# Kernel tuning notes

Hardware: AMD Instinct MI355X
Metric: run time of the kernel (lower is better)

## Reference

```python
import jax, jax.numpy as jnp
import numpy as np

B, N, F, E, K, R, H = 16, 2048, 2048, 128, 10, 2, 2


def setup_inputs() -> dict:
    key = jax.random.key(0)
    ks = jax.random.split(key, 11)
    s = 0.1  # keep embeddings close so the Gaussian kernel does not underflow
    rel = jax.random.normal(ks[0], (B, E), jnp.float32) * s
    arg1 = jax.random.normal(ks[1], (B, E), jnp.float32) * s
    arg2 = jax.random.normal(ks[2], (B, E), jnp.float32) * s
    fact_rel = jax.random.normal(ks[3], (B, F, E), jnp.float32) * s
    fact_arg1 = jax.random.normal(ks[4], (B, F, E), jnp.float32) * s
    fact_arg2 = jax.random.normal(ks[5], (B, F, E), jnp.float32) * s
    entity_embeddings = jax.random.normal(ks[6], (B, N, E), jnp.float32) * s
    hop_W = jax.random.normal(ks[7], (R, H, E, E), jnp.float32) / jnp.sqrt(jnp.float32(E))
    hop_b = jax.random.normal(ks[8], (R, H, E), jnp.float32) * 0.01
    nb_facts = jax.random.randint(ks[9], (B,), F // 2, F + 1, jnp.int32)
    nb_entities = jax.random.randint(ks[10], (B,), N // 2, N + 1, jnp.int32)
    return dict(rel=rel, arg1=arg1, arg2=arg2, fact_rel=fact_rel,
                fact_arg1=fact_arg1, fact_arg2=fact_arg2,
                entity_embeddings=entity_embeddings, hop_W=hop_W, hop_b=hop_b,
                nb_facts=nb_facts, nb_entities=nb_entities)


def reference(rel, arg1, arg2, fact_rel, fact_arg1, fact_arg2,
              entity_embeddings, hop_W, hop_b, nb_facts, nb_entities):
    # Gaussian kernel k(x,y) = exp(-||x-y||^2 / 2), batched: x [B,T,E], y [B,F,E] -> [B,T,F]
    def kern(x, y):
        d2 = (jnp.sum(x * x, -1)[:, :, None] + jnp.sum(y * y, -1)[:, None, :]
              - 2.0 * jnp.einsum('bte,bfe->btf', x, y))
        return jnp.exp(-0.5 * d2)

    fact_mask = (jnp.arange(F) < nb_facts[:, None])[:, None, :]            # [B,1,F]
    ent_mask = (jnp.arange(N) < nb_entities[:, None]).astype(rel.dtype)    # [B,N]

    # BatchNeuralKB.score: max over (valid) facts of product of kernels. [B,T,E]x3 -> [B,T]
    def model_score(r, a1, a2):
        s = kern(r, fact_rel) * kern(a1, fact_arg1) * kern(a2, fact_arg2)  # [B,T,F]
        return jnp.max(jnp.where(fact_mask, s, 0.0), axis=-1)

    # BatchNeuralKB.forward, (s,p,?) -> score per candidate object entity. [B,1,E] -> [B,N]
    def forward_sp(r, a1):
        kr = jnp.where(fact_mask, kern(r, fact_rel) * kern(a1, fact_arg1), 0.0)  # [B,1,F]
        kE = kern(entity_embeddings, fact_arg2)                                  # [B,N,F]
        return jnp.max(kr * kE, axis=-1) * ent_mask                              # [B,N]

    # (?,p,o) -> score per candidate subject entity
    def forward_po(r, a2):
        kr = jnp.where(fact_mask, kern(r, fact_rel) * kern(a2, fact_arg2), 0.0)
        kE = kern(entity_embeddings, fact_arg1)
        return jnp.max(kr * kE, axis=-1) * ent_mask

    # r_score(depth=1) = max(depth_r_score(0), depth_r_score(1))
    # depth_r_score(0) == model.score
    scores_0 = model_score(rel[:, None], arg1[:, None], arg2[:, None])[:, 0]  # [B]

    global_res = None
    for r_idx in range(R):
        is_rev = (r_idx % 2 == 1)
        # LinearReformulator: hop relations from rel
        h1 = rel @ hop_W[r_idx, 0] + hop_b[r_idx, 0]  # [B,E]
        h2 = rel @ hop_W[r_idx, 1] + hop_b[r_idx, 1]
        # hop 1: r_hop -> scores over all entities, then top-k beam
        if is_rev:
            sp = forward_po(h1[:, None], arg1[:, None])  # [B,N]
        else:
            sp = forward_sp(h1[:, None], arg1[:, None])
        z_scores, z_idx = jax.lax.top_k(sp, K)                                  # [B,K]
        z_emb = jnp.take_along_axis(entity_embeddings, z_idx[:, :, None], axis=1)  # [B,K,E]
        # final hop: r_score(depth=0) == model.score with branched args
        h2k = jnp.broadcast_to(h2[:, None, :], (B, K, E))
        a2k = jnp.broadcast_to(arg2[:, None, :], (B, K, E))
        if is_rev:
            s2 = model_score(h2k, a2k, z_emb)  # [B,K]
        else:
            s2 = model_score(h2k, z_emb, a2k)
        rule_scores = jnp.minimum(s2, z_scores)   # tnorm = 'min'
        rule_res = jnp.max(rule_scores, axis=1)   # max over branches [B]
        global_res = rule_res if global_res is None else jnp.maximum(global_res, rule_res)

    return jnp.maximum(scores_0, global_res)
```

## Files before the change

### kernel.cpp

```cpp
#include <hip/hip_runtime.h>
#include <math.h>

#define Bb 16
#define Nn 2048
#define Ff 2048
#define Ee 128
#define Kk 10
#define S2FC 8
#define S2F (Ff / S2FC)

typedef __attribute__((ext_vector_type(8))) short short8;
typedef __attribute__((ext_vector_type(4))) float f32x4;

__device__ inline float wave_sum(float x) {
    for (int o = 32; o; o >>= 1) x += __shfl_down(x, o);
    return x;
}

__device__ inline void bsplit(float x, unsigned short& h, unsigned short& l) {
    unsigned int u = __float_as_uint(x);
    h = (unsigned short)(u >> 16);
    float hf = __uint_as_float(u & 0xFFFF0000u);
    l = (unsigned short)(__float_as_uint(x - hf) >> 16);
}

__device__ inline void atomic_fmax_pos(float* addr, float v) {
    atomicMax((unsigned int*)addr, __float_as_uint(v));
}

__global__ __launch_bounds__(256) void k_pfe(
    const float* __restrict__ rel, const float* __restrict__ arg1,
    const float* __restrict__ arg2, const float* __restrict__ frel,
    const float* __restrict__ fa1, const float* __restrict__ fa2,
    const float* __restrict__ ent, const float* __restrict__ hop_W,
    const float* __restrict__ hop_b, const int* __restrict__ nb_facts,
    unsigned short* __restrict__ B0, unsigned short* __restrict__ B1,
    float* __restrict__ ent_norm, float* __restrict__ c0, float* __restrict__ c1,
    float* __restrict__ s2b0, float* __restrict__ s2b1, float* __restrict__ out) {
    int bx = blockIdx.x;
    int tid = threadIdx.x;
    if (bx < 128) {
        int fcb = bx & 7, b = bx >> 3;
        int nbf = nb_facts[b];
        if (fcb * 256 >= nbf) {
            int f = fcb * 256 + tid;
            size_t o = (size_t)b * Ff + f;
            const float NI = -INFINITY;
            c0[o] = NI; c1[o] = NI; s2b0[o] = NI; s2b1[o] = NI;
            return;
        }
        __shared__ float q[7][Ee];
        __shared__ float bred[4];
        if (tid < 128) {
            q[0][tid] = rel[b * Ee + tid];
            q[1][tid] = arg1[b * Ee + tid];
            q[2][tid] = arg2[b * Ee + tid];
        }
        __syncthreads();
        {
            int e = tid & 127, hf = tid >> 7;
            const float* W0 = hop_W + (size_t)(hf * 2) * Ee * Ee;
            const float* W1 = W0 + (size_t)Ee * Ee;
            float a0 = hop_b[(hf * 2) * Ee + e];
            float a1 = hop_b[(hf * 2 + 1) * Ee + e];
            for (int qq = 0; qq < Ee; ++qq) {
                float rq = q[0][qq];
                a0 += rq * W0[qq * Ee + e];
                a1 += rq * W1[qq * Ee + e];
            }
            q[3 + hf][e] = a0;
            q[5 + hf][e] = a1;
        }
        __syncthreads();

        int f = fcb * 256 + tid;
        const float* pr = frel + ((size_t)b * Ff + f) * Ee;
        const float* p1 = fa1 + ((size_t)b * Ff + f) * Ee;
        const float* p2 = fa2 + ((size_t)b * Ff + f) * Ee;
        float d_rr = 0, d_a11 = 0, d_a22 = 0, d_h10 = 0, d_h11 = 0, d_h20 = 0, d_h21 = 0;
        float d_a12 = 0, d_a21 = 0, n1 = 0, n2 = 0;
#pragma unroll 8
        for (int e0 = 0; e0 < Ee; e0 += 4) {
            float4 vr4 = *(const float4*)(pr + e0);
            float4 v14 = *(const float4*)(p1 + e0);
            float4 v24 = *(const float4*)(p2 + e0);
            const float* vrp = (const float*)&vr4;
            const float* v1p = (const float*)&v14;
            const float* v2p = (const float*)&v24;
#pragma unroll
            for (int j = 0; j < 4; ++j) {
                int e = e0 + j;
                float fr = vrp[j], f1 = v1p[j], f2 = v2p[j];
                float t;
                t = q[0][e] - fr; d_rr  += t * t;
                t = q[1][e] - f1; d_a11 += t * t;
                t = q[2][e] - f2; d_a22 += t * t;
                t = q[3][e] - fr; d_h10 += t * t;
                t = q[4][e] - fr; d_h11 += t * t;
                t = q[5][e] - fr; d_h20 += t * t;
                t = q[6][e] - fr; d_h21 += t * t;
                t = q[1][e] - f2; d_a12 += t * t;
                t = q[2][e] - f1; d_a21 += t * t;
                n1 += f1 * f1; n2 += f2 * f2;
            }
        }
        bool valid = f < nbf;
        const float NI = -INFINITY;
        size_t o = (size_t)b * Ff + f;
        c0[o]   = valid ? (-0.5f * (d_h10 + d_a11 + n2)) : NI;
        c1[o]   = valid ? (-0.5f * (d_h11 + d_a12 + n1)) : NI;
        s2b0[o] = valid ? (-0.5f * (d_h20 + d_a22)) : NI;
        s2b1[o] = valid ? (-0.5f * (d_h21 + d_a21)) : NI;
        float lsc = valid ? (-0.5f * (d_rr + d_a11 + d_a22)) : NI;
        for (int m = 32; m; m >>= 1) lsc = fmaxf(lsc, __shfl_down(lsc, m));
        if ((tid & 63) == 0) bred[tid >> 6] = lsc;
        __syncthreads();
        if (tid == 0) {
            float m = fmaxf(fmaxf(bred[0], bred[1]), fmaxf(bred[2], bred[3]));
            atomic_fmax_pos(out + b, expf(m));
        }
    } else if (bx < 128 + 4096) {
        int bxx = bx - 128;
        int y = bxx >> 11, bxi = bxx & 2047;
        int oct = tid & 15, fl = tid >> 4;
        int b = bxi >> 7, f = (bxi & 127) * 16 + fl;
        const float* src = (y == 0) ? fa2 : fa1;
        unsigned short* dst = ((y == 0) ? B0 : B1) +
                              (((size_t)b * 16 + oct) * Ff + f) * 16;
        const float* s = src + ((size_t)b * Ff + f) * Ee + oct * 8;
        float4 v0 = *(const float4*)s;
        float4 v1 = *(const float4*)(s + 4);
        float xs[8] = {v0.x, v0.y, v0.z, v0.w, v1.x, v1.y, v1.z, v1.w};
        unsigned short hi[8], lo[8];
#pragma unroll
        for (int j = 0; j < 8; ++j) bsplit(xs[j], hi[j], lo[j]);
        uint4 ph, pl;
        ph.x = (unsigned)hi[0] | ((unsigned)hi[1] << 16);
        ph.y = (unsigned)hi[2] | ((unsigned)hi[3] << 16);
        ph.z = (unsigned)hi[4] | ((unsigned)hi[5] << 16);
        ph.w = (unsigned)hi[6] | ((unsigned)hi[7] << 16);
        pl.x = (unsigned)lo[0] | ((unsigned)lo[1] << 16);
        pl.y = (unsigned)lo[2] | ((unsigned)lo[3] << 16);
        pl.z = (unsigned)lo[4] | ((unsigned)lo[5] << 16);
        pl.w = (unsigned)lo[6] | ((unsigned)lo[7] << 16);
        *(uint4*)dst = ph;
        *(uint4*)(dst + 8) = pl;
    } else {
        int row  = (bx - (128 + 4096)) * 4 + (tid >> 6);
        int lane = tid & 63;
        const float* p = ent + (size_t)row * Ee;
        float a = p[lane], c = p[lane + 64];
        float s = wave_sum(a * a + c * c);
        if (lane == 0) ent_norm[row] = s;
    }
}

#define BMs 128

__global__ __launch_bounds__(256, 2) void k_spmax_mfma(
    const float* __restrict__ ent, const unsigned short* __restrict__ B0,
    const unsigned short* __restrict__ B1, const float* __restrict__ c0,
    const float* __restrict__ c1, const float* __restrict__ ent_norm,
    const int* __restrict__ nb_facts, const int* __restrict__ nb_entities,
    float* __restrict__ sp0, float* __restrict__ sp1) {
    int bid = blockIdx.x;
    int br = bid & 31, nblk = bid >> 5;
    int b = br >> 1, r = br & 1;
    const unsigned short* Bt = (r == 0) ? B0 : B1;
    const float* cb = ((r == 0) ? c0 : c1) + (size_t)b * Ff;
    float* sp = ((r == 0) ? sp0 : sp1) + (size_t)b * Nn;

    int tid = threadIdx.x;
    int ne = nb_entities[b];
    if (nblk * BMs >= ne) {
        if (tid < BMs) sp[nblk * BMs + tid] = 0.0f;
        return;
    }
    int nch = (nb_facts[b] + 63) >> 6;

    __shared__ unsigned short alds[2 * 4 * 4 * 64 * 8];

    int wave = tid >> 6, lane = tid & 63;
    int wm = wave >> 1, wn = wave & 1;
    int lane15 = lane & 15, quad = lane >> 4;

    short8 ah[4][4];
    {
        const float* abase = ent + ((size_t)b * Nn + (size_t)nblk * BMs + wm * 64) * Ee;
#pragma unroll
        for (int i = 0; i < 4; ++i)
#pragma unroll
            for (int ks = 0; ks < 4; ++ks) {
                const float* p = abase + (size_t)(i * 16 + lane15) * Ee + ks * 32 + quad * 8;
                float4 v0 = *(const float4*)p;
                float4 v1 = *(const float4*)(p + 4);
                float xs[8] = {v0.x, v0.y, v0.z, v0.w, v1.x, v1.y, v1.z, v1.w};
                short8 hi8, lo8;
#pragma unroll
                for (int j = 0; j < 8; ++j) {
                    unsigned short hh, ll;
                    bsplit(xs[j], hh, ll);
                    hi8[j] = (short)hh;
                    lo8[j] = (short)ll;
                }
                ah[i][ks] = hi8;
                if (wn == 0)
                    *(short8*)&alds[(((wm * 4 + i) * 4 + ks) * 64 + lane) * 8] = lo8;
            }
    }
    __syncthreads();

    const unsigned short* bbase =
        Bt + ((((size_t)b * 16 + quad) * Ff) + wn * 32 + lane15) * 16;

    short8 pbh0[4], pbl0[4], pbh1[4], pbl1[4];
#pragma unroll
    for (int ks = 0; ks < 4; ++ks) {
        const unsigned short* p0 = bbase + ((size_t)ks * 4 * Ff) * 16;
        pbh0[ks] = *(const short8*)p0;
        pbl0[ks] = *(const short8*)(p0 + 8);
        pbh1[ks] = *(const short8*)(p0 + 256);
        pbl1[ks] = *(const short8*)(p0 + 264);
    }
    short8 bufA[4], bufB[4];
#pragma unroll
    for (int i = 0; i < 4; ++i)
        bufA[i] = *(short8*)&alds[(((wm * 4 + i) * 4 + 0) * 64 + lane) * 8];

    float mmax[4][4];
#pragma unroll
    for (int i = 0; i < 4; ++i)
#pragma unroll
        for (int rr = 0; rr < 4; ++rr) mmax[i][rr] = -INFINITY;

    for (int c = 0; c < nch; ++c) {
        int f0 = c * 64;
        float cj0 = cb[f0 + wn * 32 + lane15];
        float cj1 = cb[f0 + wn * 32 + 16 + lane15];
        f32x4 acc[4][2];
#pragma unroll
        for (int i = 0; i < 4; ++i) {
            acc[i][0] = (f32x4){cj0, cj0, cj0, cj0};
            acc[i][1] = (f32x4){cj1, cj1, cj1, cj1};
        }
        int fn = (c + 1 < nch ? c + 1 : 0) * 64;

#pragma unroll
        for (int ks = 0; ks < 4; ++ks) {
            short8 bh0 = pbh0[ks], bl0 = pbl0[ks], bh1 = pbh1[ks], bl1 = pbl1[ks];
            const unsigned short* p0 = bbase + ((size_t)ks * 4 * Ff + fn) * 16;
            pbh0[ks] = *(const short8*)p0;
            pbl0[ks] = *(const short8*)(p0 + 8);
            pbh1[ks] = *(const short8*)(p0 + 256);
            pbl1[ks] = *(const short8*)(p0 + 264);
            short8* cur = (ks & 1) ? bufB : bufA;
            short8* nxt = (ks & 1) ? bufA : bufB;
            int nks = (ks + 1) & 3;
#pragma unroll
            for (int i = 0; i < 4; ++i)
                nxt[i] = *(short8*)&alds[(((wm * 4 + i) * 4 + nks) * 64 + lane) * 8];
#pragma unroll
            for (int i = 0; i < 4; ++i) {
                acc[i][0] = __builtin_amdgcn_mfma_f32_16x16x32_bf16(ah[i][ks], bh0, acc[i][0], 0, 0, 0);
                acc[i][0] = __builtin_amdgcn_mfma_f32_16x16x32_bf16(cur[i],    bh0, acc[i][0], 0, 0, 0);
                acc[i][0] = __builtin_amdgcn_mfma_f32_16x16x32_bf16(ah[i][ks], bl0, acc[i][0], 0, 0, 0);
                acc[i][1] = __builtin_amdgcn_mfma_f32_16x16x32_bf16(ah[i][ks], bh1, acc[i][1], 0, 0, 0);
                acc[i][1] = __builtin_amdgcn_mfma_f32_16x16x32_bf16(cur[i],    bh1, acc[i][1], 0, 0, 0);
                acc[i][1] = __builtin_amdgcn_mfma_f32_16x16x32_bf16(ah[i][ks], bl1, acc[i][1], 0, 0, 0);
            }
        }

#pragma unroll
        for (int j = 0; j < 2; ++j)
#pragma unroll
            for (int i = 0; i < 4; ++i)
#pragma unroll
                for (int rr = 0; rr < 4; ++rr)
                    mmax[i][rr] = fmaxf(mmax[i][rr], acc[i][j][rr]);
    }

    __syncthreads();
    float* red = (float*)alds;
#pragma unroll
    for (int i = 0; i < 4; ++i)
#pragma unroll
        for (int rr = 0; rr < 4; ++rr) {
            float v = mmax[i][rr];
#pragma unroll
            for (int m = 1; m < 16; m <<= 1) v = fmaxf(v, __shfl_xor(v, m));
            if (lane15 == 0) red[(wm * 64 + i * 16 + quad * 4 + rr) * 2 + wn] = v;
        }
    __syncthreads();
    if (tid < BMs) {
        float m = fmaxf(red[tid * 2], red[tid * 2 + 1]);
        int n = nblk * BMs + tid;
        float v = (n < ne) ? expf(m - 0.5f * ent_norm[(size_t)b * Nn + n]) : 0.0f;
        sp[n] = v;
    }
}

__global__ __launch_bounds__(256) void k_s2t(
    const float* __restrict__ ent, const float* __restrict__ fa1,
    const float* __restrict__ fa2, const float* __restrict__ s2b0,
    const float* __restrict__ s2b1, const float* __restrict__ sp0,
    const float* __restrict__ sp1, const int* __restrict__ nb_facts,
    float* __restrict__ out) {
    int fc = blockIdx.x, b = blockIdx.y, r = blockIdx.z;
    if (fc * S2F >= nb_facts[b]) return;
    const float* factX = (r == 0) ? fa1 : fa2;
    const float* s2b   = ((r == 0) ? s2b0 : s2b1) + (size_t)b * Ff;
    const float* sp    = ((r == 0) ? sp0 : sp1) + (size_t)b * Nn;

    __shared__ float zsc[Kk];
    __shared__ int   zidx[Kk];
    __shared__ float zsh[Kk][Ee];
    __shared__ float znorm[Kk];
    __shared__ float red[4][Kk];
    __shared__ float rules[Kk];

    int tid = threadIdx.x;
    int wv = tid >> 6, lane = tid & 63;

    if (wv == 0) {
        float v[Nn / 64];
#pragma unroll
        for (int i = 0; i < Nn / 64; ++i) v[i] = sp[i * 64 + lane];
        for (int k = 0; k < Kk; ++k) {
            float best = -INFINITY; int bidx = 0;
#pragma unroll
            for (int i = 0; i < Nn / 64; ++i)
                if (v[i] > best) { best = v[i]; bidx = i * 64 + lane; }
#pragma unroll
            for (int m = 1; m < 64; m <<= 1) {
                float ov = __shfl_xor(best, m);
                int oi = __shfl_xor(bidx, m);
                if (ov > best || (ov == best && oi < bidx)) { best = ov; bidx = oi; }
            }
            if (lane == 0) { zsc[k] = best; zidx[k] = bidx; }
            if ((bidx & 63) == lane) {
                int slot = bidx >> 6;
#pragma unroll
                for (int i = 0; i < Nn / 64; ++i)
                    if (i == slot) v[i] = -INFINITY;
            }
        }
    }
    __syncthreads();
    for (int idx = tid; idx < Kk * Ee; idx += 256) {
        int k = idx >> 7, e = idx & 127;
        zsh[k][e] = ent[((size_t)b * Nn + zidx[k]) * Ee + e];
    }
    __syncthreads();
    if (tid < Kk) {
        float s = 0.f;
        for (int e = 0; e < Ee; ++e) { float v = zsh[tid][e]; s += v * v; }
        znorm[tid] = s;
    }
    __syncthreads();

    int f = fc * S2F + tid;
    const float* fp = factX + ((size_t)b * Ff + f) * Ee;
    float acc[Kk];
#pragma unroll
    for (int k = 0; k < Kk; ++k) acc[k] = 0.f;
    float nf = 0.f;
#pragma unroll 4
    for (int e0 = 0; e0 < Ee; e0 += 4) {
        float4 v = *(const float4*)(fp + e0);
        nf += v.x * v.x + v.y * v.y + v.z * v.z + v.w * v.w;
#pragma unroll
        for (int k = 0; k < Kk; ++k) {
            float4 z = *(const float4*)&zsh[k][e0];
            acc[k] += z.x * v.x + z.y * v.y + z.z * v.z + z.w * v.w;
        }
    }
    float base = s2b[f] - 0.5f * nf;
    float sc[Kk];
#pragma unroll
    for (int k = 0; k < Kk; ++k) sc[k] = base + acc[k] - 0.5f * znorm[k];
    for (int o = 32; o; o >>= 1)
#pragma unroll
        for (int k = 0; k < Kk; ++k) sc[k] = fmaxf(sc[k], __shfl_down(sc[k], o));
    if ((tid & 63) == 0)
#pragma unroll
        for (int k = 0; k < Kk; ++k) red[wv][k] = sc[k];
    __syncthreads();
    if (tid < Kk) {
        float m = fmaxf(fmaxf(red[0][tid], red[1][tid]), fmaxf(red[2][tid], red[3][tid]));
        rules[tid] = fminf(expf(m), zsc[tid]);
    }
    __syncthreads();
    if (tid == 0) {
        float g = rules[0];
#pragma unroll
        for (int k = 1; k < Kk; ++k) g = fmaxf(g, rules[k]);
        atomic_fmax_pos(out + b, g);
    }
}

extern "C" void kernel_launch(void* const* d_in, const int* in_sizes, int n_in,
                              void* d_out, int out_size, void* d_ws, size_t ws_size,
                              hipStream_t stream) {
    const float* rel  = (const float*)d_in[0];
    const float* arg1 = (const float*)d_in[1];
    const float* arg2 = (const float*)d_in[2];
    const float* frel = (const float*)d_in[3];
    const float* fa1  = (const float*)d_in[4];
    const float* fa2  = (const float*)d_in[5];
    const float* ent  = (const float*)d_in[6];
    const float* hopW = (const float*)d_in[7];
    const float* hopb = (const float*)d_in[8];
    const int* nb_facts    = (const int*)d_in[9];
    const int* nb_entities = (const int*)d_in[10];
    float* out = (float*)d_out;

    float* ws = (float*)d_ws;
    size_t off = 0;
    float* c0       = ws + off; off += (size_t)Bb * Ff;
    float* c1       = ws + off; off += (size_t)Bb * Ff;
    float* s2b0     = ws + off; off += (size_t)Bb * Ff;
    float* s2b1     = ws + off; off += (size_t)Bb * Ff;
    float* sp0      = ws + off; off += (size_t)Bb * Nn;
    float* sp1      = ws + off; off += (size_t)Bb * Nn;
    float* ent_norm = ws + off; off += (size_t)Bb * Nn;
    off = (off + 7) & ~(size_t)7;
    unsigned short* B0 = (unsigned short*)(ws + off); off += (size_t)Bb * 16 * Ff * 8;
    unsigned short* B1 = (unsigned short*)(ws + off); off += (size_t)Bb * 16 * Ff * 8;

    hipMemsetAsync(d_out, 0, (size_t)out_size * sizeof(float), stream);
    k_pfe<<<dim3(128 + 4096 + Bb * Nn / 4), 256, 0, stream>>>(
        rel, arg1, arg2, frel, fa1, fa2, ent, hopW, hopb, nb_facts,
        B0, B1, ent_norm, c0, c1, s2b0, s2b1, out);
    k_spmax_mfma<<<dim3(512), 256, 0, stream>>>(ent, B0, B1, c0, c1, ent_norm,
                                                nb_facts, nb_entities, sp0, sp1);
    k_s2t<<<dim3(S2FC, Bb, 2), 256, 0, stream>>>(ent, fa1, fa2, s2b0, s2b1,
                                                 sp0, sp1, nb_facts, out);
}
```

Baseline: 229.0 us.

## Split fact dimension across two blocks in spmax kernel with atomic max merge

The entity-vs-fact MFMA max kernel now launches twice as many blocks. Each block processes every other 64-fact chunk, and partial results are combined through an atomicMax on the float bits, which is valid because exp output is positive. sp buffers are zero-initialized in the preprocessing kernel, and launch bounds are raised to allow more occupancy. The aim is better CU utilization on a 512-block grid, at the cost of re-loading and re-splitting A tiles per block and atomic traffic.

```diff
diff --git a/kernel.cpp b/kernel.cpp
--- a/kernel.cpp
+++ b/kernel.cpp
@@ -8,6 +8,7 @@
 #define Kk 10
 #define S2FC 8
 #define S2F (Ff / S2FC)
+#define FS 2
 
 typedef __attribute__((ext_vector_type(8))) short short8;
 typedef __attribute__((ext_vector_type(4))) float f32x4;
@@ -36,7 +37,8 @@
     const float* __restrict__ hop_b, const int* __restrict__ nb_facts,
     unsigned short* __restrict__ B0, unsigned short* __restrict__ B1,
     float* __restrict__ ent_norm, float* __restrict__ c0, float* __restrict__ c1,
-    float* __restrict__ s2b0, float* __restrict__ s2b1, float* __restrict__ out) {
+    float* __restrict__ s2b0, float* __restrict__ s2b1,
+    float* __restrict__ sp0, float* __restrict__ sp1, float* __restrict__ out) {
     int bx = blockIdx.x;
     int tid = threadIdx.x;
     if (bx < 128) {
@@ -151,20 +153,24 @@
         const float* p = ent + (size_t)row * Ee;
         float a = p[lane], c = p[lane + 64];
         float s = wave_sum(a * a + c * c);
-        if (lane == 0) ent_norm[row] = s;
+        if (lane == 0) {
+            ent_norm[row] = s;
+            sp0[row] = 0.0f;
+            sp1[row] = 0.0f;
+        }
     }
 }
 
 #define BMs 128
 
-__global__ __launch_bounds__(256, 2) void k_spmax_mfma(
+__global__ __launch_bounds__(256, 4) void k_spmax_mfma(
     const float* __restrict__ ent, const unsigned short* __restrict__ B0,
     const unsigned short* __restrict__ B1, const float* __restrict__ c0,
     const float* __restrict__ c1, const float* __restrict__ ent_norm,
     const int* __restrict__ nb_facts, const int* __restrict__ nb_entities,
     float* __restrict__ sp0, float* __restrict__ sp1) {
     int bid = blockIdx.x;
-    int br = bid & 31, nblk = bid >> 5;
+    int br = bid & 31, nblk = (bid >> 5) & 15, h = bid >> 9;
     int b = br >> 1, r = br & 1;
     const unsigned short* Bt = (r == 0) ? B0 : B1;
     const float* cb = ((r == 0) ? c0 : c1) + (size_t)b * Ff;
@@ -172,11 +178,9 @@
 
     int tid = threadIdx.x;
     int ne = nb_entities[b];
-    if (nblk * BMs >= ne) {
-        if (tid < BMs) sp[nblk * BMs + tid] = 0.0f;
-        return;
-    }
+    if (nblk * BMs >= ne) return;
     int nch = (nb_facts[b] + 63) >> 6;
+    if (h >= nch) return;
 
     __shared__ unsigned short alds[2 * 4 * 4 * 64 * 8];
 
@@ -216,7 +220,7 @@
     short8 pbh0[4], pbl0[4], pbh1[4], pbl1[4];
 #pragma unroll
     for (int ks = 0; ks < 4; ++ks) {
-        const unsigned short* p0 = bbase + ((size_t)ks * 4 * Ff) * 16;
+        const unsigned short* p0 = bbase + ((size_t)ks * 4 * Ff + h * 64) * 16;
         pbh0[ks] = *(const short8*)p0;
         pbl0[ks] = *(const short8*)(p0 + 8);
         pbh1[ks] = *(const short8*)(p0 + 256);
@@ -233,7 +237,7 @@
 #pragma unroll
         for (int rr = 0; rr < 4; ++rr) mmax[i][rr] = -INFINITY;
 
-    for (int c = 0; c < nch; ++c) {
+    for (int c = h; c < nch; c += FS) {
         int f0 = c * 64;
         float cj0 = cb[f0 + wn * 32 + lane15];
         float cj1 = cb[f0 + wn * 32 + 16 + lane15];
@@ -243,7 +247,7 @@
             acc[i][0] = (f32x4){cj0, cj0, cj0, cj0};
             acc[i][1] = (f32x4){cj1, cj1, cj1, cj1};
         }
-        int fn = (c + 1 < nch ? c + 1 : 0) * 64;
+        int fn = ((c + FS < nch) ? (c + FS) : h) * 64;
 
 #pragma unroll
         for (int ks = 0; ks < 4; ++ks) {
@@ -294,8 +298,8 @@
     if (tid < BMs) {
         float m = fmaxf(red[tid * 2], red[tid * 2 + 1]);
         int n = nblk * BMs + tid;
-        float v = (n < ne) ? expf(m - 0.5f * ent_norm[(size_t)b * Nn + n]) : 0.0f;
-        sp[n] = v;
+        if (n < ne)
+            atomic_fmax_pos(&sp[n], expf(m - 0.5f * ent_norm[(size_t)b * Nn + n]));
     }
 }
 
@@ -430,9 +434,9 @@
     hipMemsetAsync(d_out, 0, (size_t)out_size * sizeof(float), stream);
     k_pfe<<<dim3(128 + 4096 + Bb * Nn / 4), 256, 0, stream>>>(
         rel, arg1, arg2, frel, fa1, fa2, ent, hopW, hopb, nb_facts,
-        B0, B1, ent_norm, c0, c1, s2b0, s2b1, out);
-    k_spmax_mfma<<<dim3(512), 256, 0, stream>>>(ent, B0, B1, c0, c1, ent_norm,
-                                                nb_facts, nb_entities, sp0, sp1);
+        B0, B1, ent_norm, c0, c1, s2b0, s2b1, sp0, sp1, out);
+    k_spmax_mfma<<<dim3(512 * FS), 256, 0, stream>>>(ent, B0, B1, c0, c1, ent_norm,
+                                                     nb_facts, nb_entities, sp0, sp1);
     k_s2t<<<dim3(S2FC, Bb, 2), 256, 0, stream>>>(ent, fa1, fa2, s2b0, s2b1,
                                                  sp0, sp1, nb_facts, out);
 }
```

New measurement: 360.8 us. 1.58x slower.
